# Kernel tuning notes

Hardware: AMD Instinct MI355X
Metric: run time of the kernel (lower is better)

The kernel has to match this reference:

```python
import jax, jax.numpy as jnp
import numpy as np

B, N, D = 8, 1024, 256
H, DK, DV = 8, 64, 64
NEG = -1.0e9


def setup_inputs() -> dict:
    key = jax.random.key(0)
    ks = jax.random.split(key, 8)
    node_features = jax.random.normal(ks[0], (B, N, D), dtype=jnp.float32)
    em = (jax.random.uniform(ks[1], (B, 1, N, N)) < 0.03).astype(jnp.float32)
    eye = jnp.eye(N, dtype=jnp.float32)[None, None]
    edge_mask = jnp.maximum(em, eye)
    distance_weights = jax.random.uniform(ks[2], (B, N), dtype=jnp.float32)
    s = 1.0 / np.sqrt(D)
    Wq = jax.random.normal(ks[3], (D, H * DK), dtype=jnp.float32) * s
    Wk = jax.random.normal(ks[4], (D, H * DK), dtype=jnp.float32) * s
    Wv = jax.random.normal(ks[5], (D, H * DV), dtype=jnp.float32) * s
    Wo = jax.random.normal(ks[6], (H * DV, D), dtype=jnp.float32) / np.sqrt(H * DV)
    bo = jnp.zeros((D,), dtype=jnp.float32)
    return {"node_features": node_features, "edge_mask": edge_mask,
            "distance_weights": distance_weights,
            "Wq": Wq, "Wk": Wk, "Wv": Wv, "Wo": Wo, "bo": bo}


def reference(node_features, edge_mask, distance_weights, Wq, Wk, Wv, Wo, bo):
    b, n, d = node_features.shape
    # project and split heads: [B, H, N, dk]
    q = (node_features @ Wq).reshape(b, n, H, DK).transpose(0, 2, 1, 3)
    k = (node_features @ Wk).reshape(b, n, H, DK).transpose(0, 2, 1, 3)
    v = (node_features @ Wv).reshape(b, n, H, DV).transpose(0, 2, 1, 3)
    # scaled dot-product logits [B, H, N, N]
    logits = jnp.einsum('bhsd,bhtd->bhst', q, k) / jnp.sqrt(jnp.float32(DK))
    # additive edge-mask bias (masked pairs pushed to -1e9)
    logits = logits + (1.0 - edge_mask) * NEG
    # multiplicative per-key distance modulation
    logits = logits * distance_weights[:, None, None, :]
    w = jax.nn.softmax(logits, axis=-1)
    out = jnp.einsum('bhst,bhtd->bhsd', w, v)
    out = out.transpose(0, 2, 1, 3).reshape(b, n, H * DV)
    return out @ Wo + bo
```

## Files before the change

kernel.cpp:

```cpp
#include <hip/hip_runtime.h>
#include <hip/hip_bf16.h>
#include <hip/hip_fp16.h>
#include <cstdint>

#define B_ 8
#define N_ 1024
#define D_ 256
#define H_ 8
#define HD_ 512

typedef _Float16 f16;
typedef _Float16 f16x8 __attribute__((ext_vector_type(8)));
typedef _Float16 f16x4 __attribute__((ext_vector_type(4)));
typedef float f32x4 __attribute__((ext_vector_type(4)));
typedef unsigned long long ull;
typedef unsigned long long ull2 __attribute__((ext_vector_type(2)));

__device__ __forceinline__ void gload16(const void* g, void* l) {
    __builtin_amdgcn_global_load_lds(
        (const __attribute__((address_space(1))) unsigned int*)(uintptr_t)g,
        (__attribute__((address_space(3))) unsigned int*)(uintptr_t)l,
        16, 0, 0);
}

template<int RN>
__device__ __forceinline__ float rowror(float x) {
    return __builtin_bit_cast(float, __builtin_amdgcn_mov_dpp(
        __builtin_bit_cast(int, x), 0x120 + RN, 0xf, 0xf, true));
}
__device__ __forceinline__ float rowmax16(float x) {
    x = fmaxf(x, rowror<1>(x)); x = fmaxf(x, rowror<2>(x));
    x = fmaxf(x, rowror<4>(x)); x = fmaxf(x, rowror<8>(x));
    return x;
}
__device__ __forceinline__ float rowsum16(float x) {
    x += rowror<1>(x); x += rowror<2>(x);
    x += rowror<4>(x); x += rowror<8>(x);
    return x;
}

__global__ __launch_bounds__(256) void pre_kernel(
    const float* __restrict__ mask, ull* __restrict__ bmT,
    const float* __restrict__ Wq, const float* __restrict__ Wk,
    const float* __restrict__ Wv, f16* __restrict__ WT,
    const float* __restrict__ X, f16* __restrict__ Xh)
{
    __shared__ float Ws[64][65];
    const int bid = blockIdx.x;
    const int tid = threadIdx.x;
    if (bid < 2048) {
        const int wv = tid >> 6, lane = tid & 63;
        const int r = bid * 4 + wv;
        const int b = r >> 10, n = r & 1023;
        const float* row = mask + ((size_t)b * N_ + n) * N_;
        for (int tt = 0; tt < 16; ++tt) {
            float v = row[tt * 64 + lane];
            ull m = __ballot(v != 0.0f);
            if (lane == 0) bmT[((size_t)b * 16 + tt) * N_ + n] = m;
        }
    } else if (bid < 2144) {
        const int t = bid - 2048;
        const int c0 = (t % 24) * 64, k0 = (t / 24) * 64;
        const int m = c0 >> 9, cw0 = c0 & 511;
        const float* Wsel = (m == 0) ? Wq : (m == 1) ? Wk : Wv;
        const float scale = (m == 0) ? 0.125f : 1.0f;
        const int rr = tid >> 6, cc = tid & 63;
        for (int i = 0; i < 16; ++i)
            Ws[i * 4 + rr][cc] = Wsel[(size_t)(k0 + i * 4 + rr) * HD_ + cw0 + cc];
        __syncthreads();
        for (int i = 0; i < 16; ++i)
            WT[(size_t)(c0 + i * 4 + rr) * D_ + k0 + cc] =
                (f16)(Ws[cc][i * 4 + rr] * scale);
    } else {
        const size_t i = (size_t)((bid - 2144) * 256 + tid) * 4;
        f32x4 v = *reinterpret_cast<const f32x4*>(X + i);
        f16x4 h2;
        for (int j = 0; j < 4; ++j) h2[j] = (f16)v[j];
        *reinterpret_cast<f16x4*>(Xh + i) = h2;
    }
}

__global__ __launch_bounds__(256) void wconv_o_kernel(
    const float* __restrict__ Wo, f16* __restrict__ WToT)
{
    __shared__ float Ws[64][65];
    const int tid = threadIdx.x;
    const int c0 = blockIdx.x * 64, k0 = blockIdx.y * 64;
    const int rr = tid >> 6, cc = tid & 63;
    for (int i = 0; i < 16; ++i)
        Ws[i * 4 + rr][cc] = Wo[(size_t)(k0 + i * 4 + rr) * D_ + c0 + cc];
    __syncthreads();
    for (int i = 0; i < 16; ++i)
        WToT[(size_t)(c0 + i * 4 + rr) * HD_ + k0 + cc] = (f16)Ws[cc][i * 4 + rr];
}

__global__ __launch_bounds__(256, 3) void qkv_kernel(
    const f16* __restrict__ Xh, const f16* __restrict__ WT,
    f16* __restrict__ Qh, f16* __restrict__ Kh, f16* __restrict__ Vt)
{
    __shared__ f16 Ash[2][4096];
    __shared__ f16 Wsh[2][8192];
    const int tid = threadIdx.x;
    const int wv = tid >> 6, lane = tid & 63;
    const int g = lane >> 4, li = lane & 15;
    const int row0 = blockIdx.x * 64;
    const int c0 = blockIdx.y * 128;
    const int m = c0 >> 9, cw0 = c0 & 511;

    f32x4 acc[4][2] = {};

    auto stage = [&](int ks, int bf) {
        for (int i = 0; i < 2; ++i) {
            const int idx = i * 256 + tid;
            const int r = idx >> 3, ch = idx & 7;
            const f16* src = Xh + (size_t)(row0 + r) * D_ + ks * 64 + ((ch ^ (r & 7)) * 8);
            gload16(src, &Ash[bf][idx * 8]);
        }
        for (int i = 0; i < 4; ++i) {
            const int idx = i * 256 + tid;
            const int c = idx >> 3, ch = idx & 7;
            const f16* src = WT + (size_t)(c0 + c) * D_ + ks * 64 + ((ch ^ (c & 7)) * 8);
            gload16(src, &Wsh[bf][idx * 8]);
        }
    };
    stage(0, 0);
    __syncthreads();
    int bf = 0;
    for (int ks = 0; ks < 4; ++ks) {
        if (ks < 3) stage(ks + 1, bf ^ 1);
        for (int kk = 0; kk < 2; ++kk) {
            f16x8 af[4];
            for (int rf = 0; rf < 4; ++rf) {
                const int r = rf * 16 + li;
                af[rf] = *reinterpret_cast<const f16x8*>(
                    &Ash[bf][r * 64 + (((kk * 4 + g) ^ (r & 7)) * 8)]);
            }
            __builtin_amdgcn_s_setprio(1);
            for (int cf = 0; cf < 2; ++cf) {
                const int cl = wv * 32 + cf * 16 + li;
                f16x8 bm_ = *reinterpret_cast<const f16x8*>(
                    &Wsh[bf][cl * 64 + (((kk * 4 + g) ^ (cl & 7)) * 8)]);
                for (int rf = 0; rf < 4; ++rf)
                    acc[rf][cf] = __builtin_amdgcn_mfma_f32_16x16x32_f16(
                        af[rf], bm_, acc[rf][cf], 0, 0, 0);
            }
            __builtin_amdgcn_s_setprio(0);
        }
        __syncthreads();
        bf ^= 1;
    }
    const int b = row0 >> 10;
    for (int cf = 0; cf < 2; ++cf) {
        const int cw = cw0 + wv * 32 + cf * 16 + li;
        const int h = cw >> 6, dk = cw & 63;
        for (int rf = 0; rf < 4; ++rf) {
            const int nloc = (row0 & 1023) + rf * 16 + g * 4;
            if (m < 2) {
                f16* dst = (m == 0 ? Qh : Kh) + ((size_t)(b * H_ + h) * N_ + nloc) * 64 + dk;
                for (int j = 0; j < 4; ++j) dst[(size_t)j * 64] = (f16)acc[rf][cf][j];
            } else {
                f16x4 v4;
                for (int j = 0; j < 4; ++j) v4[j] = (f16)acc[rf][cf][j];
                *reinterpret_cast<f16x4*>(
                    Vt + ((size_t)(b * H_ + h) * 64 + dk) * N_ + nloc) = v4;
            }
        }
    }
}

__global__ __launch_bounds__(256, 4) void attn_kernel(
    const f16* __restrict__ Qh, const f16* __restrict__ Kh,
    const f16* __restrict__ Vt,
    const ull* __restrict__ bm, const float* __restrict__ dw,
    f16* __restrict__ AO)
{
    __shared__ f16 Ksh[8192];
    __shared__ f16 Vsh[8192];
    const int tid = threadIdx.x;
    const int wv = tid >> 6, lane = tid & 63;
    const int g = lane >> 4, li = lane & 15;
    const int bid = (blockIdx.x & 7) * 128 + (blockIdx.x >> 3);
    const int st = bid & 15, h = (bid >> 4) & 7, b = bid >> 7;
    const int s0 = st * 64 + wv * 16;

    const f16* Qbase = Qh + (size_t)(b * H_ + h) * N_ * 64;
    const f16* Kbase = Kh + (size_t)(b * H_ + h) * N_ * 64;
    const f16* Vbase = Vt + (size_t)(b * H_ + h) * 64 * N_;

    f16x8 qf0 = *reinterpret_cast<const f16x8*>(Qbase + (size_t)(s0 + li) * 64 + g * 8);
    f16x8 qf1 = *reinterpret_cast<const f16x8*>(Qbase + (size_t)(s0 + li) * 64 + 32 + g * 8);

    int ro0[4], ro1[4];
    for (int fc = 0; fc < 4; ++fc) {
        const int r = fc * 16 + li;
        ro0[fc] = r * 64 + ((g ^ (r & 7)) * 8);
        ro1[fc] = r * 64 + (((4 | g) ^ (r & 7)) * 8);
    }
    int pw[4][4];
    for (int fc = 0; fc < 4; ++fc)
        for (int j = 0; j < 4; ++j) {
            const int r = g * 4 + j;
            const int R = (r < 8) ? (8 * wv + r) : (24 + 8 * wv + r);
            pw[fc][j] = R * 64 + (((fc * 2 + (li >> 3)) ^ (R & 7)) * 8) + (li & 7);
        }
    const int Rli = (li < 8) ? (8 * wv + li) : (24 + 8 * wv + li);
    const int pr0 = Rli * 64 + ((g ^ (Rli & 7)) * 8);
    const int pr1 = Rli * 64 + (((4 | g) ^ (Rli & 7)) * 8);

    const int s0i = wv * 64 + lane, s1i = 256 + wv * 64 + lane;
    const int r0_ = s0i >> 3, c0_ = ((s0i & 7) ^ (r0_ & 7)) * 8;
    const int r1_ = s1i >> 3, c1_ = ((s1i & 7) ^ (r1_ & 7)) * 8;
    const f16* kp0 = Kbase + r0_ * 64 + c0_;
    const f16* kp1 = Kbase + r1_ * 64 + c1_;
    const f16* vp0 = Vbase + (size_t)r0_ * N_ + c0_;
    const f16* vp1 = Vbase + (size_t)r1_ * N_ + c1_;
    f16* const kd0 = Ksh + s0i * 8;
    f16* const kd1 = Ksh + s1i * 8;
    f16* const vd0 = Vsh + s0i * 8;
    f16* const vd1 = Vsh + s1i * 8;

    const ull* bmp = bm + (size_t)b * 16 * N_ + s0 + g * 4;
    const float* dwp = dw + b * N_ + li;

    f32x4 of[4] = {};
    float m_run[4], l_run[4];
    for (int j = 0; j < 4; ++j) { m_run[j] = -1e30f; l_run[j] = 0.f; }

    gload16(kp0, kd0); gload16(kp1, kd1);
    gload16(vp0, vd0); gload16(vp1, vd1);
    kp0 += 4096; kp1 += 4096; vp0 += 64; vp1 += 64;
    __syncthreads();
    int koff = 0;

    for (int tt = 0; tt < 16; ++tt) {
        const int nb = koff ^ 4096;
        if (tt < 15) {
            gload16(kp0, kd0 + nb); gload16(kp1, kd1 + nb);
            kp0 += 4096; kp1 += 4096;
        }
        ull2 w01 = *reinterpret_cast<const ull2*>(bmp);
        ull2 w23 = *reinterpret_cast<const ull2*>(bmp + 2);
        bmp += N_;
        float dwc[4], bdw[4];
        for (int fc = 0; fc < 4; ++fc) {
            dwc[fc] = dwp[fc * 16] * 1.442695041f;
            bdw[fc] = dwc[fc] * -1.0e9f;
        }
        dwp += 64;

        f32x4 s[4] = {};
        __builtin_amdgcn_s_setprio(1);
        for (int fc = 0; fc < 4; ++fc) {
            f16x8 kf0 = *reinterpret_cast<const f16x8*>(Ksh + koff + ro0[fc]);
            f16x8 kf1 = *reinterpret_cast<const f16x8*>(Ksh + koff + ro1[fc]);
            s[fc] = __builtin_amdgcn_mfma_f32_16x16x32_f16(qf0, kf0, s[fc], 0, 0, 0);
            s[fc] = __builtin_amdgcn_mfma_f32_16x16x32_f16(qf1, kf1, s[fc], 0, 0, 0);
        }
        __builtin_amdgcn_s_setprio(0);

        ull wsh[4];
        wsh[0] = w01.x >> li; wsh[1] = w01.y >> li;
        wsh[2] = w23.x >> li; wsh[3] = w23.y >> li;

        float mt[4] = {-1e30f, -1e30f, -1e30f, -1e30f};
        for (int fc = 0; fc < 4; ++fc)
            for (int j = 0; j < 4; ++j) {
                const float sel = ((wsh[j] >> (fc * 16)) & 1ull) ? 0.0f : bdw[fc];
                const float lg = fmaf(s[fc][j], dwc[fc], sel);
                s[fc][j] = lg;
                mt[j] = fmaxf(mt[j], lg);
            }
        for (int j = 0; j < 4; ++j) mt[j] = rowmax16(mt[j]);

        const bool small = (mt[0] - m_run[0] <= 8.f) & (mt[1] - m_run[1] <= 8.f) &
                           (mt[2] - m_run[2] <= 8.f) & (mt[3] - m_run[3] <= 8.f);
        if (!__all(small)) {
            for (int j = 0; j < 4; ++j) {
                const float mn = fmaxf(m_run[j], mt[j]);
                const float alpha = __builtin_amdgcn_exp2f(m_run[j] - mn);
                m_run[j] = mn;
                l_run[j] *= alpha;
                for (int fc = 0; fc < 4; ++fc) of[fc][j] *= alpha;
            }
        }
        float rs[4] = {0.f, 0.f, 0.f, 0.f};
        for (int fc = 0; fc < 4; ++fc)
            for (int j = 0; j < 4; ++j) {
                const float p = __builtin_amdgcn_exp2f(s[fc][j] - m_run[j]);
                s[fc][j] = p;
                rs[j] += p;
            }
        for (int j = 0; j < 4; ++j)
            l_run[j] += rowsum16(rs[j]);

        {
            f16* vnb = Vsh + nb;
            for (int fc = 0; fc < 4; ++fc)
                for (int j = 0; j < 4; ++j)
                    vnb[pw[fc][j]] = (f16)s[fc][j];
            f16x8 pf0 = *reinterpret_cast<const f16x8*>(vnb + pr0);
            f16x8 pf1 = *reinterpret_cast<const f16x8*>(vnb + pr1);
            asm volatile("s_waitcnt lgkmcnt(0)" ::: "memory");
            __builtin_amdgcn_sched_barrier(0);
            if (tt < 15) {
                gload16(vp0, vd0 + nb); gload16(vp1, vd1 + nb);
                vp0 += 64; vp1 += 64;
            }
            __builtin_amdgcn_s_setprio(1);
            for (int fc = 0; fc < 4; ++fc) {
                f16x8 vf0 = *reinterpret_cast<const f16x8*>(Vsh + koff + ro0[fc]);
                f16x8 vf1 = *reinterpret_cast<const f16x8*>(Vsh + koff + ro1[fc]);
                of[fc] = __builtin_amdgcn_mfma_f32_16x16x32_f16(pf0, vf0, of[fc], 0, 0, 0);
                of[fc] = __builtin_amdgcn_mfma_f32_16x16x32_f16(pf1, vf1, of[fc], 0, 0, 0);
            }
            __builtin_amdgcn_s_setprio(0);
        }
        __syncthreads();
        koff ^= 4096;
    }
    for (int j = 0; j < 4; ++j) {
        const float inv = 1.f / l_run[j];
        const int srow = s0 + g * 4 + j;
        f16* dst = AO + ((size_t)b * N_ + srow) * HD_ + h * 64;
        for (int fc = 0; fc < 4; ++fc)
            dst[fc * 16 + li] = (f16)(of[fc][j] * inv);
    }
}

__global__ __launch_bounds__(256, 4) void proj_kernel(
    const f16* __restrict__ AO, const f16* __restrict__ WToT,
    const float* __restrict__ bo, float* __restrict__ out)
{
    __shared__ f16 Ash[16 * 512];
    const int tid = threadIdx.x;
    const int wv = tid >> 6, lane = tid & 63;
    const int g = lane >> 4, li = lane & 15;
    const int row0 = blockIdx.x * 16;
    const int c0 = wv * 64;

    for (int i = 0; i < 4; ++i) {
        const int idx = i * 256 + tid;
        const int r = idx >> 6, ch = idx & 63;
        const f16* src = AO + (size_t)(row0 + r) * HD_ + ((ch ^ (r & 7)) * 8);
        gload16(src, &Ash[idx * 8]);
    }
    __syncthreads();

    f32x4 acc[4] = {};
    for (int k0 = 0; k0 < HD_; k0 += 32) {
        const int cb = k0 >> 3;
        f16x8 af = *reinterpret_cast<const f16x8*>(
            &Ash[li * HD_ + (((cb + g) ^ (li & 7)) * 8)]);
        for (int fc = 0; fc < 4; ++fc) {
            f16x8 bf = *reinterpret_cast<const f16x8*>(
                WToT + (size_t)(c0 + fc * 16 + li) * HD_ + k0 + g * 8);
            acc[fc] = __builtin_amdgcn_mfma_f32_16x16x32_f16(af, bf, acc[fc], 0, 0, 0);
        }
    }
    for (int fc = 0; fc < 4; ++fc) {
        const int c = c0 + fc * 16 + li;
        const float bias = bo[c];
        for (int j = 0; j < 4; ++j)
            out[(size_t)(row0 + g * 4 + j) * D_ + c] = acc[fc][j] + bias;
    }
}

extern "C" void kernel_launch(void* const* d_in, const int* in_sizes, int n_in,
                              void* d_out, int out_size, void* d_ws, size_t ws_size,
                              hipStream_t stream) {
    const float* X    = (const float*)d_in[0];
    const float* mask = (const float*)d_in[1];
    const float* dwv  = (const float*)d_in[2];
    const float* Wq   = (const float*)d_in[3];
    const float* Wk   = (const float*)d_in[4];
    const float* Wv   = (const float*)d_in[5];
    const float* Wo   = (const float*)d_in[6];
    const float* bo   = (const float*)d_in[7];
    float* out = (float*)d_out;

    const size_t per = (size_t)B_ * H_ * N_ * 64;
    f16* Qh = (f16*)d_ws;
    f16* Kh = Qh + per;
    f16* Vt = Kh + per;
    f16* AO = Vt + per;
    f16* WToT = (f16*)d_ws;

    ull* bmT   = (ull*)d_out;
    f16* WTqkv = (f16*)((char*)d_out + (1u << 20));
    f16* Xh    = (f16*)((char*)d_out + (2u << 20));

    pre_kernel<<<dim3(2048 + 96 + 2048), 256, 0, stream>>>(
        mask, bmT, Wq, Wk, Wv, WTqkv, X, Xh);
    qkv_kernel<<<dim3(128, 12), 256, 0, stream>>>(Xh, WTqkv, Qh, Kh, Vt);
    attn_kernel<<<dim3(1024), 256, 0, stream>>>(Qh, Kh, Vt, bmT, dwv, AO);
    wconv_o_kernel<<<dim3(4, 8), 256, 0, stream>>>(Wo, WToT);
    proj_kernel<<<dim3(512, 1), 256, 0, stream>>>(AO, WToT, bo, out);
}
```

Before: 182.5 us.

## Prefetch mask/distance for next tile and compute softmax row sums via MFMA

The attention loop now loads the next tile's bitmask words and distance weights during the current iteration, so their global-load latency is hidden behind the QK MFMAs. The per-row softmax denominator is accumulated with two extra MFMAs against a ones vector, replacing the DPP row-sum reductions. The sum now comes from the f16-rounded probabilities, which matches what feeds the PV product. The Wo conversion kernel is launched earlier into a separate workspace region when space allows, and the loop is unrolled by two. Costs are more registers and two extra MFMAs per tile.

```diff
diff --git a/kernel.cpp b/kernel.cpp
--- a/kernel.cpp
+++ b/kernel.cpp
@@ -31,11 +31,6 @@
 __device__ __forceinline__ float rowmax16(float x) {
     x = fmaxf(x, rowror<1>(x)); x = fmaxf(x, rowror<2>(x));
     x = fmaxf(x, rowror<4>(x)); x = fmaxf(x, rowror<8>(x));
-    return x;
-}
-__device__ __forceinline__ float rowsum16(float x) {
-    x += rowror<1>(x); x += rowror<2>(x);
-    x += rowror<4>(x); x += rowror<8>(x);
     return x;
 }
 
@@ -190,6 +185,9 @@
     f16x8 qf0 = *reinterpret_cast<const f16x8*>(Qbase + (size_t)(s0 + li) * 64 + g * 8);
     f16x8 qf1 = *reinterpret_cast<const f16x8*>(Qbase + (size_t)(s0 + li) * 64 + 32 + g * 8);
 
+    f16x8 onesv;
+    for (int j = 0; j < 8; ++j) onesv[j] = (f16)1.0f;
+
     int ro0[4], ro1[4];
     for (int fc = 0; fc < 4; ++fc) {
         const int r = fc * 16 + li;
@@ -223,31 +221,34 @@
     const float* dwp = dw + b * N_ + li;
 
     f32x4 of[4] = {};
-    float m_run[4], l_run[4];
-    for (int j = 0; j < 4; ++j) { m_run[j] = -1e30f; l_run[j] = 0.f; }
+    f32x4 ls = {};
+    float m_run[4];
+    for (int j = 0; j < 4; ++j) m_run[j] = -1e30f;
 
     gload16(kp0, kd0); gload16(kp1, kd1);
     gload16(vp0, vd0); gload16(vp1, vd1);
     kp0 += 4096; kp1 += 4096; vp0 += 64; vp1 += 64;
+
+    ull2 w01 = *reinterpret_cast<const ull2*>(bmp);
+    ull2 w23 = *reinterpret_cast<const ull2*>(bmp + 2);
+    bmp += N_;
+    float dwc[4], bdw[4];
+    for (int fc = 0; fc < 4; ++fc) {
+        dwc[fc] = dwp[fc * 16] * 1.442695041f;
+        bdw[fc] = dwc[fc] * -1.0e9f;
+    }
+    dwp += 64;
+
     __syncthreads();
     int koff = 0;
 
+    #pragma unroll 2
     for (int tt = 0; tt < 16; ++tt) {
         const int nb = koff ^ 4096;
         if (tt < 15) {
             gload16(kp0, kd0 + nb); gload16(kp1, kd1 + nb);
             kp0 += 4096; kp1 += 4096;
         }
-        ull2 w01 = *reinterpret_cast<const ull2*>(bmp);
-        ull2 w23 = *reinterpret_cast<const ull2*>(bmp + 2);
-        bmp += N_;
-        float dwc[4], bdw[4];
-        for (int fc = 0; fc < 4; ++fc) {
-            dwc[fc] = dwp[fc * 16] * 1.442695041f;
-            bdw[fc] = dwc[fc] * -1.0e9f;
-        }
-        dwp += 64;
-
         f32x4 s[4] = {};
         __builtin_amdgcn_s_setprio(1);
         for (int fc = 0; fc < 4; ++fc) {
@@ -258,6 +259,21 @@
         }
         __builtin_amdgcn_s_setprio(0);
 
+        ull2 nw01 = w01, nw23 = w23;
+        float ndwc[4], nbdw[4];
+        if (tt < 15) {
+            nw01 = *reinterpret_cast<const ull2*>(bmp);
+            nw23 = *reinterpret_cast<const ull2*>(bmp + 2);
+            bmp += N_;
+            for (int fc = 0; fc < 4; ++fc) {
+                ndwc[fc] = dwp[fc * 16] * 1.442695041f;
+                nbdw[fc] = ndwc[fc] * -1.0e9f;
+            }
+            dwp += 64;
+        } else {
+            for (int fc = 0; fc < 4; ++fc) { ndwc[fc] = 0.f; nbdw[fc] = 0.f; }
+        }
+
         ull wsh[4];
         wsh[0] = w01.x >> li; wsh[1] = w01.y >> li;
         wsh[2] = w23.x >> li; wsh[3] = w23.y >> li;
@@ -279,19 +295,13 @@
                 const float mn = fmaxf(m_run[j], mt[j]);
                 const float alpha = __builtin_amdgcn_exp2f(m_run[j] - mn);
                 m_run[j] = mn;
-                l_run[j] *= alpha;
+                ls[j] *= alpha;
                 for (int fc = 0; fc < 4; ++fc) of[fc][j] *= alpha;
             }
         }
-        float rs[4] = {0.f, 0.f, 0.f, 0.f};
         for (int fc = 0; fc < 4; ++fc)
-            for (int j = 0; j < 4; ++j) {
-                const float p = __builtin_amdgcn_exp2f(s[fc][j] - m_run[j]);
-                s[fc][j] = p;
-                rs[j] += p;
-            }
-        for (int j = 0; j < 4; ++j)
-            l_run[j] += rowsum16(rs[j]);
+            for (int j = 0; j < 4; ++j)
+                s[fc][j] = __builtin_amdgcn_exp2f(s[fc][j] - m_run[j]);
 
         {
             f16* vnb = Vsh + nb;
@@ -307,6 +317,8 @@
                 vp0 += 64; vp1 += 64;
             }
             __builtin_amdgcn_s_setprio(1);
+            ls = __builtin_amdgcn_mfma_f32_16x16x32_f16(pf0, onesv, ls, 0, 0, 0);
+            ls = __builtin_amdgcn_mfma_f32_16x16x32_f16(pf1, onesv, ls, 0, 0, 0);
             for (int fc = 0; fc < 4; ++fc) {
                 f16x8 vf0 = *reinterpret_cast<const f16x8*>(Vsh + koff + ro0[fc]);
                 f16x8 vf1 = *reinterpret_cast<const f16x8*>(Vsh + koff + ro1[fc]);
@@ -317,9 +329,11 @@
         }
         __syncthreads();
         koff ^= 4096;
+        w01 = nw01; w23 = nw23;
+        for (int fc = 0; fc < 4; ++fc) { dwc[fc] = ndwc[fc]; bdw[fc] = nbdw[fc]; }
     }
     for (int j = 0; j < 4; ++j) {
-        const float inv = 1.f / l_run[j];
+        const float inv = 1.f / ls[j];
         const int srow = s0 + g * 4 + j;
         f16* dst = AO + ((size_t)b * N_ + srow) * HD_ + h * 64;
         for (int fc = 0; fc < 4; ++fc)
@@ -383,7 +397,9 @@
     f16* Kh = Qh + per;
     f16* Vt = Kh + per;
     f16* AO = Vt + per;
-    f16* WToT = (f16*)d_ws;
+
+    const bool wsx = ws_size >= ((33ull) << 20);
+    f16* WToT = wsx ? (f16*)((char*)d_ws + ((32ull) << 20)) : (f16*)d_ws;
 
     ull* bmT   = (ull*)d_out;
     f16* WTqkv = (f16*)((char*)d_out + (1u << 20));
@@ -391,8 +407,9 @@
 
     pre_kernel<<<dim3(2048 + 96 + 2048), 256, 0, stream>>>(
         mask, bmT, Wq, Wk, Wv, WTqkv, X, Xh);
+    if (wsx) wconv_o_kernel<<<dim3(4, 8), 256, 0, stream>>>(Wo, WToT);
     qkv_kernel<<<dim3(128, 12), 256, 0, stream>>>(Xh, WTqkv, Qh, Kh, Vt);
     attn_kernel<<<dim3(1024), 256, 0, stream>>>(Qh, Kh, Vt, bmT, dwv, AO);
-    wconv_o_kernel<<<dim3(4, 8), 256, 0, stream>>>(Wo, WToT);
+    if (!wsx) wconv_o_kernel<<<dim3(4, 8), 256, 0, stream>>>(Wo, WToT);
     proj_kernel<<<dim3(512, 1), 256, 0, stream>>>(AO, WToT, bo, out);
 }
```

Measured after the change: 175.8 us. -3.6%, faster.
